# Optimization experiments

Hardware: AMD Instinct MI355X
Metric: run time of the kernel (lower is better)

## Reference

```python
import jax, jax.numpy as jnp
import numpy as np

H = 1.0  # primo_h
N_GRID = 768


def _grid_mesh(n):
    ii, jj = np.meshgrid(np.arange(n - 1), np.arange(n - 1), indexing='ij')
    v00 = (ii * n + jj).ravel(); v10 = ((ii + 1) * n + jj).ravel()
    v01 = (ii * n + jj + 1).ravel(); v11 = ((ii + 1) * n + jj + 1).ravel()
    tri1 = np.stack([v00, v10, v01], 1); tri2 = np.stack([v10, v11, v01], 1)
    return np.concatenate([tri1, tri2], 0).astype(np.int32)  # [F,3]


def _face_adjacency(faces):
    # faces: [F,3] -> edges [E,2] (sorted vertex pairs), face_ids [E,2]
    F = faces.shape[0]
    fe = np.stack([faces[:, [0, 1]], faces[:, [1, 2]], faces[:, [2, 0]]], 1).reshape(-1, 2)
    fe = np.sort(fe, axis=1)
    fid = np.repeat(np.arange(F, dtype=np.int32), 3)
    order = np.lexsort((fe[:, 1], fe[:, 0]))
    fs, fi = fe[order], fid[order]
    same = np.all(fs[:-1] == fs[1:], axis=1)
    k = np.nonzero(same)[0]
    edges = fs[k].astype(np.int32)
    face_ids = np.stack([fi[k], fi[k + 1]], 1).astype(np.int32)
    return edges, face_ids


def setup_inputs() -> dict:
    key = jax.random.key(0)
    k1, k2, k3 = jax.random.split(key, 3)
    faces_np = _grid_mesh(N_GRID)                      # [F,3]
    edges_np, face_ids_np = _face_adjacency(faces_np)  # [E,2],[E,2]
    F = faces_np.shape[0]
    V = N_GRID * N_GRID
    return {
        'transformed_prism': jax.random.normal(k1, (F, 3, 3), dtype=jnp.float32),
        'rotations': jax.random.normal(k2, (F, 3, 3), dtype=jnp.float32),
        'verts': jax.random.normal(k3, (1, V, 3), dtype=jnp.float32),
        'faces': jnp.asarray(faces_np.T),       # [3,F], matches torch forward arg
        'edges': jnp.asarray(edges_np),
        'face_ids': jnp.asarray(face_ids_np),
    }


def _verts_id_face(Ft, E, Q):
    # Ft: [F,3] faces; E: [e,2] edge vertex ids; Q: [e,2] adjacent face ids
    fa, fb = Ft[Q[:, 0]], Ft[Q[:, 1]]  # [e,3]

    def find(fv, tgt):
        return jnp.where(fv[:, 0] == tgt, 0,
               jnp.where(fv[:, 1] == tgt, 1,
               jnp.where(fv[:, 2] == tgt, 2, -1)))

    return jnp.stack([find(fa, E[:, 0]), find(fa, E[:, 1]),
                      find(fb, E[:, 0]), find(fb, E[:, 1])], axis=1)  # [e,4]


def reference(transformed_prism, rotations, verts, faces, edges, face_ids):
    tp = transformed_prism
    bs = verts.shape[0]
    v = verts.reshape(-1, 3)
    Ft = faces.T  # [F,3]

    # per-face normals (vectorized version of the original per-face loop)
    e1 = tp[:, 0] - tp[:, 1]
    e2 = tp[:, 0] - tp[:, 2]
    nrm = jnp.cross(e1, e2)
    normals = nrm / jnp.linalg.norm(nrm, axis=-1, keepdims=True)  # [F,3]

    # face areas
    p1, p2, p3 = v[Ft[:, 0]], v[Ft[:, 1]], v[Ft[:, 2]]
    face_areas = 0.5 * jnp.linalg.norm(jnp.cross(p2 - p1, p3 - p1), axis=1)

    # faithful to original: normals indexed by edge VERTEX ids
    n1, n2 = normals[edges[:, 0]], normals[edges[:, 1]]
    fid1, fid2 = face_ids[:, 0], face_ids[:, 1]
    r1, r2 = rotations[fid1], rotations[fid2]

    ftv = _verts_id_face(Ft, edges, face_ids)  # [e,4]
    v1_p1, v2_p1 = tp[fid1, ftv[:, 0]], tp[fid1, ftv[:, 1]]
    v1_p2, v2_p2 = tp[fid2, ftv[:, 2]], tp[fid2, ftv[:, 3]]

    p1n1 = jnp.einsum('ec,ecd->ed', n1, r1)
    p1n2 = jnp.einsum('ec,ecd->ed', n2, r1)
    p2n1 = jnp.einsum('ec,ecd->ed', n1, r2)
    p2n2 = jnp.einsum('ec,ecd->ed', n2, r2)

    A = jnp.stack([v1_p1 + p1n1 * H, v2_p1 + p1n2 * H,
                   v1_p1 - p1n1 * H, v2_p1 - p1n2 * H], axis=1)  # [e,4,3]
    B = jnp.stack([v1_p2 + p2n1 * H, v2_p2 + p2n2 * H,
                   v1_p2 - p2n1 * H, v2_p2 - p2n2 * H], axis=1)
    D = A - B

    # coeff[p,q] = 2^{-|i_p-i_q|-|j_p-j_q|}, (i,j) over {0,1}^2
    idx = jnp.array([[0, 0], [0, 1], [1, 0], [1, 1]], dtype=jnp.float32)
    coeff = 2.0 ** (-jnp.abs(idx[:, None] - idx[None, :]).sum(-1))  # [4,4]
    pair = jnp.einsum('epc,eqc->epq', D, D)
    energy = (pair * coeff).sum((1, 2)) / 9.0  # [e]

    weight = jnp.sum((v[edges[:, 0]] - v[edges[:, 1]]) ** 2, axis=1) \
             / (face_areas[fid1] + face_areas[fid2])
    return (energy * weight).sum() / bs
```

## Files before the change

kernel.cpp:

```cpp
#include <hip/hip_runtime.h>


#define TI 8
#define TJ 32

struct __attribute__((aligned(4))) F4s { float a, b, c, d; };
struct F3 { float x, y, z; };

__device__ __forceinline__ void load9(const float* __restrict__ p, float* d) {
    F4s u0 = *(const F4s*)p;
    F4s u1 = *(const F4s*)(p + 4);
    d[0] = u0.a; d[1] = u0.b; d[2] = u0.c; d[3] = u0.d;
    d[4] = u1.a; d[5] = u1.b; d[6] = u1.c; d[7] = u1.d;
    d[8] = p[8];
}

__device__ __forceinline__ int iclamp(int x, int lo, int hi) {
    return x < lo ? lo : (x > hi ? hi : x);
}

__device__ __forceinline__ float edge_ew(const float* u1, const float* u2,
                                         const float* w1, const float* w2,
                                         const float* rA, const float* rB,
                                         const F3& n1, const F3& n2,
                                         const F3& pa, const F3& pb,
                                         float asum) {
    float ux = u1[0] - u2[0], uy = u1[1] - u2[1], uz = u1[2] - u2[2];
    float wx = w1[0] - w2[0], wy = w1[1] - w2[1], wz = w1[2] - w2[2];

    float d0 = rA[0] - rB[0], d1 = rA[1] - rB[1], d2 = rA[2] - rB[2];
    float d3 = rA[3] - rB[3], d4 = rA[4] - rB[4], d5 = rA[5] - rB[5];
    float d6 = rA[6] - rB[6], d7 = rA[7] - rB[7], d8 = rA[8] - rB[8];

    float ax = n1.x * d0 + n1.y * d3 + n1.z * d6;
    float ay = n1.x * d1 + n1.y * d4 + n1.z * d7;
    float az = n1.x * d2 + n1.y * d5 + n1.z * d8;
    float bx = n2.x * d0 + n2.y * d3 + n2.z * d6;
    float by = n2.x * d1 + n2.y * d4 + n2.z * d7;
    float bz = n2.x * d2 + n2.y * d5 + n2.z * d8;

    float uu = ux * ux + uy * uy + uz * uz;
    float ww = wx * wx + wy * wy + wz * wz;
    float uw = ux * wx + uy * wy + uz * wz;
    float aa = ax * ax + ay * ay + az * az;
    float bb = bx * bx + by * by + bz * bz;
    float ab = ax * bx + ay * by + az * bz;
    float energy = (3.0f * (uu + ww + uw) + (aa + bb + ab)) * (1.0f / 9.0f);

    float dx = pa.x - pb.x, dy = pa.y - pb.y, dz = pa.z - pb.z;
    return energy * (dx * dx + dy * dy + dz * dz) / asum;
}

__global__ __launch_bounds__(256) void fused_kernel(
        const float* __restrict__ tp,
        const float* __restrict__ rot,
        const float* __restrict__ verts,
        double* __restrict__ partials,
        int n) {
    const int m = n - 1;
    const int Q = m * m;
    const int tid = threadIdx.x;
    const int i0 = blockIdx.y * TI;
    const int j0 = blockIdx.x * TJ;

    __shared__ float sT1[TI * TJ * 9];
    __shared__ float sR1[TI * TJ * 9];
    __shared__ float sT2[(TI + 1) * (TJ + 1) * 9];
    __shared__ float sR2[(TI + 1) * (TJ + 1) * 9];
    __shared__ float sV[(TI + 2) * (TJ + 2) * 3];
    __shared__ float sN[(TI + 1) * (TJ + 1) * 3];
    __shared__ float sA1[TI * TJ];
    __shared__ float sA2[(TI + 1) * (TJ + 1)];
    __shared__ double sred[4];

    for (int idx = tid; idx < TI * TJ * 9; idx += 256) {
        int r = idx / (TJ * 9);
        int o = idx - r * (TJ * 9);
        int k = o / 9, c = o - k * 9;
        int gi = iclamp(i0 + r, 0, m - 1);
        int gj = iclamp(j0 + k, 0, m - 1);
        size_t f = (size_t)gi * m + gj;
        sT1[idx] = tp[9 * f + c];
        sR1[idx] = rot[9 * f + c];
    }
    for (int idx = tid; idx < (TI + 1) * (TJ + 1) * 9; idx += 256) {
        int r = idx / ((TJ + 1) * 9);
        int o = idx - r * ((TJ + 1) * 9);
        int k = o / 9, c = o - k * 9;
        int gi = iclamp(i0 - 1 + r, 0, m - 1);
        int gj = iclamp(j0 - 1 + k, 0, m - 1);
        size_t f = (size_t)Q + (size_t)gi * m + gj;
        sT2[idx] = tp[9 * f + c];
        sR2[idx] = rot[9 * f + c];
    }
    for (int idx = tid; idx < (TI + 2) * (TJ + 2) * 3; idx += 256) {
        int r = idx / ((TJ + 2) * 3);
        int o = idx - r * ((TJ + 2) * 3);
        int k = o / 3, c = o - k * 3;
        int gi = iclamp(i0 - 1 + r, 0, n - 1);
        int gj = iclamp(j0 - 1 + k, 0, n - 1);
        sV[idx] = verts[3 * ((size_t)gi * n + gj) + c];
    }
    for (int v = tid; v < (TI + 1) * (TJ + 1); v += 256) {
        int vi = v / (TJ + 1), vj = v - vi * (TJ + 1);
        int gi = iclamp(i0 + vi, 0, n - 1);
        int gj = iclamp(j0 + vj, 0, n - 1);
        float r[9];
        load9(tp + 9 * ((size_t)gi * n + gj), r);
        float e1x = r[0] - r[3], e1y = r[1] - r[4], e1z = r[2] - r[5];
        float e2x = r[0] - r[6], e2y = r[1] - r[7], e2z = r[2] - r[8];
        float nx = e1y * e2z - e1z * e2y;
        float ny = e1z * e2x - e1x * e2z;
        float nz = e1x * e2y - e1y * e2x;
        float inv = 1.0f / sqrtf(nx * nx + ny * ny + nz * nz);
        sN[3 * v] = nx * inv; sN[3 * v + 1] = ny * inv; sN[3 * v + 2] = nz * inv;
    }

    __syncthreads();

    {
        int ti = tid / TJ, tj = tid - ti * TJ;
        const float* p00 = sV + 3 * ((ti + 1) * (TJ + 2) + (tj + 1));
        const float* p10 = sV + 3 * ((ti + 2) * (TJ + 2) + (tj + 1));
        const float* p01 = sV + 3 * ((ti + 1) * (TJ + 2) + (tj + 2));
        float ax = p10[0] - p00[0], ay = p10[1] - p00[1], az = p10[2] - p00[2];
        float bx = p01[0] - p00[0], by = p01[1] - p00[1], bz = p01[2] - p00[2];
        float cx = ay * bz - az * by, cy = az * bx - ax * bz, cz = ax * by - ay * bx;
        sA1[tid] = 0.5f * sqrtf(cx * cx + cy * cy + cz * cz);
    }
    for (int v = tid; v < (TI + 1) * (TJ + 1); v += 256) {
        int r = v / (TJ + 1), k = v - r * (TJ + 1);
        const float* p10 = sV + 3 * ((r + 1) * (TJ + 2) + k);
        const float* p11 = sV + 3 * ((r + 1) * (TJ + 2) + (k + 1));
        const float* p01 = sV + 3 * (r * (TJ + 2) + (k + 1));
        float ax = p11[0] - p10[0], ay = p11[1] - p10[1], az = p11[2] - p10[2];
        float bx = p01[0] - p10[0], by = p01[1] - p10[1], bz = p01[2] - p10[2];
        float cx = ay * bz - az * by, cy = az * bx - ax * bz, cz = ax * by - ay * bx;
        sA2[v] = 0.5f * sqrtf(cx * cx + cy * cy + cz * cz);
    }

    __syncthreads();

    int ti = tid / TJ, tj = tid - ti * TJ;
    int i = i0 + ti, j = j0 + tj;
    double term = 0.0;
    if (i < m && j < m) {
        const float* t1 = sT1 + 9 * tid;
        const float* r1 = sR1 + 9 * tid;
        const float* t2c = sT2 + 9 * ((ti + 1) * (TJ + 1) + (tj + 1));
        const float* r2c = sR2 + 9 * ((ti + 1) * (TJ + 1) + (tj + 1));
        float a1 = sA1[tid];

        F3 nA = { sN[3 * (ti * (TJ + 1) + tj)],
                  sN[3 * (ti * (TJ + 1) + tj) + 1],
                  sN[3 * (ti * (TJ + 1) + tj) + 2] };
        F3 nB = { sN[3 * (ti * (TJ + 1) + tj + 1)],
                  sN[3 * (ti * (TJ + 1) + tj + 1) + 1],
                  sN[3 * (ti * (TJ + 1) + tj + 1) + 2] };
        F3 nC = { sN[3 * ((ti + 1) * (TJ + 1) + tj)],
                  sN[3 * ((ti + 1) * (TJ + 1) + tj) + 1],
                  sN[3 * ((ti + 1) * (TJ + 1) + tj) + 2] };
        const float* pv00 = sV + 3 * ((ti + 1) * (TJ + 2) + (tj + 1));
        const float* pv01 = sV + 3 * ((ti + 1) * (TJ + 2) + (tj + 2));
        const float* pv10 = sV + 3 * ((ti + 2) * (TJ + 2) + (tj + 1));
        F3 pA = { pv00[0], pv00[1], pv00[2] };
        F3 pB = { pv01[0], pv01[1], pv01[2] };
        F3 pC = { pv10[0], pv10[1], pv10[2] };

        float sum = 0.0f;
        sum += edge_ew(t1 + 6, t2c + 6, t1 + 3, t2c + 0, r1, r2c,
                       nB, nC, pB, pC, a1 + sA2[(ti + 1) * (TJ + 1) + (tj + 1)]);
        if (i > 0) {
            const float* th = sT2 + 9 * (ti * (TJ + 1) + (tj + 1));
            const float* rh = sR2 + 9 * (ti * (TJ + 1) + (tj + 1));
            sum += edge_ew(t1 + 0, th + 0, t1 + 6, th + 3, r1, rh,
                           nA, nB, pA, pB, a1 + sA2[ti * (TJ + 1) + (tj + 1)]);
        }
        if (j > 0) {
            const float* tv = sT2 + 9 * ((ti + 1) * (TJ + 1) + tj);
            const float* rv = sR2 + 9 * ((ti + 1) * (TJ + 1) + tj);
            sum += edge_ew(t1 + 0, tv + 6, t1 + 3, tv + 3, r1, rv,
                           nA, nC, pA, pC, a1 + sA2[(ti + 1) * (TJ + 1) + tj]);
        }
        term = (double)sum;
    }

#pragma unroll
    for (int off = 32; off > 0; off >>= 1) term += __shfl_down(term, off, 64);
    int lane = tid & 63, wid = tid >> 6;
    if (lane == 0) sred[wid] = term;
    __syncthreads();
    if (tid == 0) {
        partials[blockIdx.y * gridDim.x + blockIdx.x] =
            sred[0] + sred[1] + sred[2] + sred[3];
    }
}

__global__ __launch_bounds__(256) void finalize_kernel(
        const double* __restrict__ partials, int P, float* __restrict__ out) {
    double s = 0.0;
    for (int i = threadIdx.x; i < P; i += 256) s += partials[i];
#pragma unroll
    for (int off = 32; off > 0; off >>= 1) s += __shfl_down(s, off, 64);
    __shared__ double sred[4];
    int lane = threadIdx.x & 63, wid = threadIdx.x >> 6;
    if (lane == 0) sred[wid] = s;
    __syncthreads();
    if (threadIdx.x == 0) out[0] = (float)(sred[0] + sred[1] + sred[2] + sred[3]);
}

extern "C" void kernel_launch(void* const* d_in, const int* in_sizes, int n_in,
                              void* d_out, int out_size, void* d_ws, size_t ws_size,
                              hipStream_t stream) {
    const float* tp    = (const float*)d_in[0];
    const float* rot   = (const float*)d_in[1];
    const float* verts = (const float*)d_in[2];

    int V = in_sizes[2] / 3;
    int n = (int)(sqrtf((float)V) + 0.5f);
    int m = n - 1;

    double* partials = (double*)d_ws;
    float*  out      = (float*)d_out;

    dim3 grid((m + TJ - 1) / TJ, (m + TI - 1) / TI);
    int P = grid.x * grid.y;
    fused_kernel<<<grid, 256, 0, stream>>>(tp, rot, verts, partials, n);
    finalize_kernel<<<1, 256, 0, stream>>>(partials, P, out);
}
```

Before: 180.7 us.

## Replace shared-memory tiled halo staging with direct per-thread global loads

Drops the 2D tiled kernel that staged prism, rotation, vertex, normal and area data into shared memory with halos. Each thread now handles one quad on a 1D grid and loads its neighbours' data straight from global memory, recomputing normals and areas in registers. This removes the large LDS footprint, the strided scalar gather loops and the barriers. In exchange, neighbouring threads read overlapping data redundantly and the loads are strided by 9 floats per thread, so the kernel relies on L1/L2 caching to absorb the duplication.

```diff
diff --git a/kernel.cpp b/kernel.cpp
--- a/kernel.cpp
+++ b/kernel.cpp
@@ -1,22 +1,48 @@
 #include <hip/hip_runtime.h>
 
 
-#define TI 8
-#define TJ 32
-
 struct __attribute__((aligned(4))) F4s { float a, b, c, d; };
 struct F3 { float x, y, z; };
+struct R9 { float v[9]; };
+struct R6 { float v[6]; };
 
-__device__ __forceinline__ void load9(const float* __restrict__ p, float* d) {
+__device__ __forceinline__ R9 load9(const float* __restrict__ p) {
+    R9 r;
     F4s u0 = *(const F4s*)p;
     F4s u1 = *(const F4s*)(p + 4);
-    d[0] = u0.a; d[1] = u0.b; d[2] = u0.c; d[3] = u0.d;
-    d[4] = u1.a; d[5] = u1.b; d[6] = u1.c; d[7] = u1.d;
-    d[8] = p[8];
+    r.v[0] = u0.a; r.v[1] = u0.b; r.v[2] = u0.c; r.v[3] = u0.d;
+    r.v[4] = u1.a; r.v[5] = u1.b; r.v[6] = u1.c; r.v[7] = u1.d;
+    r.v[8] = p[8];
+    return r;
 }
 
-__device__ __forceinline__ int iclamp(int x, int lo, int hi) {
-    return x < lo ? lo : (x > hi ? hi : x);
+__device__ __forceinline__ R6 load6(const float* __restrict__ p) {
+    R6 r;
+    F4s u = *(const F4s*)p;
+    r.v[0] = u.a; r.v[1] = u.b; r.v[2] = u.c; r.v[3] = u.d;
+    r.v[4] = p[4]; r.v[5] = p[5];
+    return r;
+}
+
+__device__ __forceinline__ F3 load3(const float* __restrict__ p) {
+    F3 r; r.x = p[0]; r.y = p[1]; r.z = p[2]; return r;
+}
+
+__device__ __forceinline__ F3 normal_of(const R9& r) {
+    float e1x = r.v[0] - r.v[3], e1y = r.v[1] - r.v[4], e1z = r.v[2] - r.v[5];
+    float e2x = r.v[0] - r.v[6], e2y = r.v[1] - r.v[7], e2z = r.v[2] - r.v[8];
+    float nx = e1y * e2z - e1z * e2y;
+    float ny = e1z * e2x - e1x * e2z;
+    float nz = e1x * e2y - e1y * e2x;
+    float inv = 1.0f / sqrtf(nx * nx + ny * ny + nz * nz);
+    F3 o; o.x = nx * inv; o.y = ny * inv; o.z = nz * inv; return o;
+}
+
+__device__ __forceinline__ float tri_area(const F3& p, const F3& q, const F3& r) {
+    float ax = q.x - p.x, ay = q.y - p.y, az = q.z - p.z;
+    float bx = r.x - p.x, by = r.y - p.y, bz = r.z - p.z;
+    float cx = ay * bz - az * by, cy = az * bx - ax * bz, cz = ax * by - ay * bx;
+    return 0.5f * sqrtf(cx * cx + cy * cy + cz * cz);
 }
 
 __device__ __forceinline__ float edge_ew(const float* u1, const float* u2,
@@ -60,140 +86,65 @@
     const int m = n - 1;
     const int Q = m * m;
     const int tid = threadIdx.x;
-    const int i0 = blockIdx.y * TI;
-    const int j0 = blockIdx.x * TJ;
+    int q = blockIdx.x * 256 + tid;
+    bool valid = q < Q;
+    int qc = valid ? q : Q - 1;
+    int i = qc / m;
+    int j = qc - i * m;
 
-    __shared__ float sT1[TI * TJ * 9];
-    __shared__ float sR1[TI * TJ * 9];
-    __shared__ float sT2[(TI + 1) * (TJ + 1) * 9];
-    __shared__ float sR2[(TI + 1) * (TJ + 1) * 9];
-    __shared__ float sV[(TI + 2) * (TJ + 2) * 3];
-    __shared__ float sN[(TI + 1) * (TJ + 1) * 3];
-    __shared__ float sA1[TI * TJ];
-    __shared__ float sA2[(TI + 1) * (TJ + 1)];
-    __shared__ double sred[4];
+    int v00 = i * n + j;
+    R9 tA = load9(tp + (size_t)9 * v00);
+    R9 tB = load9(tp + (size_t)9 * (v00 + 1));
+    R9 tC = load9(tp + (size_t)9 * (v00 + n));
+    F3 p00 = load3(verts + (size_t)3 * v00);
+    F3 p01 = load3(verts + (size_t)3 * (v00 + 1));
+    F3 p10 = load3(verts + (size_t)3 * (v00 + n));
+    F3 p11 = load3(verts + (size_t)3 * (v00 + n + 1));
+    int iu = (i > 0) ? (i - 1) : 0;
+    int jl = (j > 0) ? (j - 1) : 0;
+    F3 pup = load3(verts + (size_t)3 * ((size_t)iu * n + (j + 1)));
+    F3 plf = load3(verts + (size_t)3 * ((size_t)(i + 1) * n + jl));
 
-    for (int idx = tid; idx < TI * TJ * 9; idx += 256) {
-        int r = idx / (TJ * 9);
-        int o = idx - r * (TJ * 9);
-        int k = o / 9, c = o - k * 9;
-        int gi = iclamp(i0 + r, 0, m - 1);
-        int gj = iclamp(j0 + k, 0, m - 1);
-        size_t f = (size_t)gi * m + gj;
-        sT1[idx] = tp[9 * f + c];
-        sR1[idx] = rot[9 * f + c];
-    }
-    for (int idx = tid; idx < (TI + 1) * (TJ + 1) * 9; idx += 256) {
-        int r = idx / ((TJ + 1) * 9);
-        int o = idx - r * ((TJ + 1) * 9);
-        int k = o / 9, c = o - k * 9;
-        int gi = iclamp(i0 - 1 + r, 0, m - 1);
-        int gj = iclamp(j0 - 1 + k, 0, m - 1);
-        size_t f = (size_t)Q + (size_t)gi * m + gj;
-        sT2[idx] = tp[9 * f + c];
-        sR2[idx] = rot[9 * f + c];
-    }
-    for (int idx = tid; idx < (TI + 2) * (TJ + 2) * 3; idx += 256) {
-        int r = idx / ((TJ + 2) * 3);
-        int o = idx - r * ((TJ + 2) * 3);
-        int k = o / 3, c = o - k * 3;
-        int gi = iclamp(i0 - 1 + r, 0, n - 1);
-        int gj = iclamp(j0 - 1 + k, 0, n - 1);
-        sV[idx] = verts[3 * ((size_t)gi * n + gj) + c];
-    }
-    for (int v = tid; v < (TI + 1) * (TJ + 1); v += 256) {
-        int vi = v / (TJ + 1), vj = v - vi * (TJ + 1);
-        int gi = iclamp(i0 + vi, 0, n - 1);
-        int gj = iclamp(j0 + vj, 0, n - 1);
-        float r[9];
-        load9(tp + 9 * ((size_t)gi * n + gj), r);
-        float e1x = r[0] - r[3], e1y = r[1] - r[4], e1z = r[2] - r[5];
-        float e2x = r[0] - r[6], e2y = r[1] - r[7], e2z = r[2] - r[8];
-        float nx = e1y * e2z - e1z * e2y;
-        float ny = e1z * e2x - e1x * e2z;
-        float nz = e1x * e2y - e1y * e2x;
-        float inv = 1.0f / sqrtf(nx * nx + ny * ny + nz * nz);
-        sN[3 * v] = nx * inv; sN[3 * v + 1] = ny * inv; sN[3 * v + 2] = nz * inv;
-    }
+    int f1  = i * m + j;
+    int f2c = Q + f1;
+    int f2u = Q + iu * m + j;
+    int f2l = Q + i * m + jl;
+    R9 t1 = load9(tp  + (size_t)9 * f1);
+    R9 t2 = load9(tp  + (size_t)9 * f2c);
+    R9 r1 = load9(rot + (size_t)9 * f1);
+    R9 r2 = load9(rot + (size_t)9 * f2c);
+    R6 th = load6(tp  + (size_t)9 * f2u);
+    R9 rh = load9(rot + (size_t)9 * f2u);
+    R6 tv = load6(tp  + (size_t)9 * f2l + 3);
+    R9 rv = load9(rot + (size_t)9 * f2l);
 
-    __syncthreads();
+    F3 nA = normal_of(tA);
+    F3 nB = normal_of(tB);
+    F3 nC = normal_of(tC);
+    float a1    = tri_area(p00, p10, p01);
+    float a2c   = tri_area(p10, p11, p01);
+    float a2up  = tri_area(p00, p01, pup);
+    float a2lf  = tri_area(plf, p10, p00);
 
-    {
-        int ti = tid / TJ, tj = tid - ti * TJ;
-        const float* p00 = sV + 3 * ((ti + 1) * (TJ + 2) + (tj + 1));
-        const float* p10 = sV + 3 * ((ti + 2) * (TJ + 2) + (tj + 1));
-        const float* p01 = sV + 3 * ((ti + 1) * (TJ + 2) + (tj + 2));
-        float ax = p10[0] - p00[0], ay = p10[1] - p00[1], az = p10[2] - p00[2];
-        float bx = p01[0] - p00[0], by = p01[1] - p00[1], bz = p01[2] - p00[2];
-        float cx = ay * bz - az * by, cy = az * bx - ax * bz, cz = ax * by - ay * bx;
-        sA1[tid] = 0.5f * sqrtf(cx * cx + cy * cy + cz * cz);
-    }
-    for (int v = tid; v < (TI + 1) * (TJ + 1); v += 256) {
-        int r = v / (TJ + 1), k = v - r * (TJ + 1);
-        const float* p10 = sV + 3 * ((r + 1) * (TJ + 2) + k);
-        const float* p11 = sV + 3 * ((r + 1) * (TJ + 2) + (k + 1));
-        const float* p01 = sV + 3 * (r * (TJ + 2) + (k + 1));
-        float ax = p11[0] - p10[0], ay = p11[1] - p10[1], az = p11[2] - p10[2];
-        float bx = p01[0] - p10[0], by = p01[1] - p10[1], bz = p01[2] - p10[2];
-        float cx = ay * bz - az * by, cy = az * bx - ax * bz, cz = ax * by - ay * bx;
-        sA2[v] = 0.5f * sqrtf(cx * cx + cy * cy + cz * cz);
-    }
+    float sum = edge_ew(t1.v + 6, t2.v + 6, t1.v + 3, t2.v + 0, r1.v, r2.v,
+                        nB, nC, p01, p10, a1 + a2c);
+    float eh = edge_ew(t1.v + 0, th.v + 0, t1.v + 6, th.v + 3, r1.v, rh.v,
+                       nA, nB, p00, p01, a1 + a2up);
+    float ev = edge_ew(t1.v + 0, tv.v + 3, t1.v + 3, tv.v + 0, r1.v, rv.v,
+                       nA, nC, p00, p10, a1 + a2lf);
+    sum += (i > 0 ? eh : 0.0f);
+    sum += (j > 0 ? ev : 0.0f);
 
-    __syncthreads();
-
-    int ti = tid / TJ, tj = tid - ti * TJ;
-    int i = i0 + ti, j = j0 + tj;
-    double term = 0.0;
-    if (i < m && j < m) {
-        const float* t1 = sT1 + 9 * tid;
-        const float* r1 = sR1 + 9 * tid;
-        const float* t2c = sT2 + 9 * ((ti + 1) * (TJ + 1) + (tj + 1));
-        const float* r2c = sR2 + 9 * ((ti + 1) * (TJ + 1) + (tj + 1));
-        float a1 = sA1[tid];
-
-        F3 nA = { sN[3 * (ti * (TJ + 1) + tj)],
-                  sN[3 * (ti * (TJ + 1) + tj) + 1],
-                  sN[3 * (ti * (TJ + 1) + tj) + 2] };
-        F3 nB = { sN[3 * (ti * (TJ + 1) + tj + 1)],
-                  sN[3 * (ti * (TJ + 1) + tj + 1) + 1],
-                  sN[3 * (ti * (TJ + 1) + tj + 1) + 2] };
-        F3 nC = { sN[3 * ((ti + 1) * (TJ + 1) + tj)],
-                  sN[3 * ((ti + 1) * (TJ + 1) + tj) + 1],
-                  sN[3 * ((ti + 1) * (TJ + 1) + tj) + 2] };
-        const float* pv00 = sV + 3 * ((ti + 1) * (TJ + 2) + (tj + 1));
-        const float* pv01 = sV + 3 * ((ti + 1) * (TJ + 2) + (tj + 2));
-        const float* pv10 = sV + 3 * ((ti + 2) * (TJ + 2) + (tj + 1));
-        F3 pA = { pv00[0], pv00[1], pv00[2] };
-        F3 pB = { pv01[0], pv01[1], pv01[2] };
-        F3 pC = { pv10[0], pv10[1], pv10[2] };
-
-        float sum = 0.0f;
-        sum += edge_ew(t1 + 6, t2c + 6, t1 + 3, t2c + 0, r1, r2c,
-                       nB, nC, pB, pC, a1 + sA2[(ti + 1) * (TJ + 1) + (tj + 1)]);
-        if (i > 0) {
-            const float* th = sT2 + 9 * (ti * (TJ + 1) + (tj + 1));
-            const float* rh = sR2 + 9 * (ti * (TJ + 1) + (tj + 1));
-            sum += edge_ew(t1 + 0, th + 0, t1 + 6, th + 3, r1, rh,
-                           nA, nB, pA, pB, a1 + sA2[ti * (TJ + 1) + (tj + 1)]);
-        }
-        if (j > 0) {
-            const float* tv = sT2 + 9 * ((ti + 1) * (TJ + 1) + tj);
-            const float* rv = sR2 + 9 * ((ti + 1) * (TJ + 1) + tj);
-            sum += edge_ew(t1 + 0, tv + 6, t1 + 3, tv + 3, r1, rv,
-                           nA, nC, pA, pC, a1 + sA2[(ti + 1) * (TJ + 1) + tj]);
-        }
-        term = (double)sum;
-    }
+    double term = valid ? (double)sum : 0.0;
 
 #pragma unroll
     for (int off = 32; off > 0; off >>= 1) term += __shfl_down(term, off, 64);
+    __shared__ double sred[4];
     int lane = tid & 63, wid = tid >> 6;
     if (lane == 0) sred[wid] = term;
     __syncthreads();
-    if (tid == 0) {
-        partials[blockIdx.y * gridDim.x + blockIdx.x] =
-            sred[0] + sred[1] + sred[2] + sred[3];
-    }
+    if (tid == 0)
+        partials[blockIdx.x] = sred[0] + sred[1] + sred[2] + sred[3];
 }
 
 __global__ __launch_bounds__(256) void finalize_kernel(
@@ -219,12 +170,12 @@
     int V = in_sizes[2] / 3;
     int n = (int)(sqrtf((float)V) + 0.5f);
     int m = n - 1;
+    int Q = m * m;
 
     double* partials = (double*)d_ws;
     float*  out      = (float*)d_out;
 
-    dim3 grid((m + TJ - 1) / TJ, (m + TI - 1) / TI);
-    int P = grid.x * grid.y;
-    fused_kernel<<<grid, 256, 0, stream>>>(tp, rot, verts, partials, n);
+    int P = (Q + 255) / 256;
+    fused_kernel<<<P, 256, 0, stream>>>(tp, rot, verts, partials, n);
     finalize_kernel<<<1, 256, 0, stream>>>(partials, P, out);
 }
```

Result: faster. 155.6 us (-13.9%).
